# Kernel tuning notes

Measured on AMD Instinct MI355X. Metric: run time of the kernel, lower is better.

Reference implementation:

```python
import jax, jax.numpy as jnp
import numpy as np

NEG_SLOPE = 0.2  # LeakyReLU negative slope (act_negative)


def setup_inputs() -> dict:
    key = jax.random.key(0)
    ks = jax.random.split(key, 5)
    B, N, D = 64, 4096, 16
    x = jax.random.normal(ks[0], (B, N, D), dtype=jnp.float32)
    # random adjacency, scaled so row sums are O(1) and activations stay stable
    adj = jax.random.uniform(ks[1], (N, N), dtype=jnp.float32) * (2.0 / N)
    Identity = jnp.eye(N, dtype=jnp.float32)
    W0 = jax.random.normal(ks[2], (D, D), dtype=jnp.float32) * (1.0 / np.sqrt(D))
    W1 = jax.random.normal(ks[3], (D, D), dtype=jnp.float32) * (1.0 / np.sqrt(D))
    W2 = jax.random.normal(ks[4], (D, D), dtype=jnp.float32) * (1.0 / np.sqrt(D))
    return {"x": x, "adj": adj, "Identity": Identity, "W0": W0, "W1": W1, "W2": W2}


def _gcn_layer(x, W, adj, I):
    # GCNConv: linear (no bias) -> leaky_relu -> batched adjacency matmul.
    # The same conv (same W) is applied with adj and with Identity, then summed.
    h = jax.nn.leaky_relu(jnp.einsum('bnd,de->bne', x, W), NEG_SLOPE)
    out_adj = jnp.einsum('nm,bmh->bnh', adj, h)  # replaces per-sample torch.mm loop
    out_id = jnp.einsum('nm,bmh->bnh', I, h)
    return out_adj + out_id


def reference(x, adj, Identity, W0, W1, W2):
    out = _gcn_layer(x, W0, adj, Identity)
    out = _gcn_layer(out, W1, adj, Identity)
    out = _gcn_layer(out, W2, adj, Identity)
    return out  # is_residual=False: no shortcut branch
```

## Files before the change

### kernel.cpp

```cpp
#include <hip/hip_runtime.h>
#include <stdint.h>


typedef float  f32x4  __attribute__((ext_vector_type(4)));
typedef unsigned short ushort8 __attribute__((ext_vector_type(8)));
typedef int    i32x4  __attribute__((ext_vector_type(4)));
typedef int    i32x8  __attribute__((ext_vector_type(8)));

typedef __attribute__((address_space(1))) void* as1p;
typedef __attribute__((address_space(3))) void* as3p;
#define GLOAD_LDS16(G, L) \
  __builtin_amdgcn_global_load_lds((as1p)(G), (as3p)(L), 16, 0, 0)

#define P_ELEMS 4194304
#define ADJ_SCALE 4096.0f
#define ADJ_DESCALE (1.0f / 4096.0f)
#define SCALE_ONE 0x7f7f7f7f

__device__ __forceinline__ unsigned short f2bf(float f) {
  unsigned u = __float_as_uint(f);
  u += 0x7fffu + ((u >> 16) & 1u);
  return (unsigned short)(u >> 16);
}
__device__ __forceinline__ float bf2f(unsigned short u) {
  return __uint_as_float(((unsigned)u) << 16);
}
__device__ __forceinline__ int pk4_fp8(float a, float b, float c, float d) {
  int v = __builtin_amdgcn_cvt_pk_fp8_f32(a, b, 0, false);
  v = __builtin_amdgcn_cvt_pk_fp8_f32(c, d, v, true);
  return v;
}

__global__ void prep(const float* __restrict__ adj,
                     unsigned char* __restrict__ a8,
                     const float* __restrict__ x,
                     const float* __restrict__ W,
                     unsigned char* __restrict__ hb8,
                     unsigned short* __restrict__ hnc_out) {
  __shared__ float xs[64 * 65];
  __shared__ unsigned short ht[64 * 72];
  int bid = blockIdx.x;

  if (bid >= 1024) {
    size_t base = ((size_t)(bid - 1024) * 256 + threadIdx.x) * 16;
    const float4* src = (const float4*)(adj + base);
    float4 q0 = src[0], q1 = src[1], q2 = src[2], q3 = src[3];
    int4 o;
    o.x = pk4_fp8(q0.x * ADJ_SCALE, q0.y * ADJ_SCALE, q0.z * ADJ_SCALE, q0.w * ADJ_SCALE);
    o.y = pk4_fp8(q1.x * ADJ_SCALE, q1.y * ADJ_SCALE, q1.z * ADJ_SCALE, q1.w * ADJ_SCALE);
    o.z = pk4_fp8(q2.x * ADJ_SCALE, q2.y * ADJ_SCALE, q2.z * ADJ_SCALE, q2.w * ADJ_SCALE);
    o.w = pk4_fp8(q3.x * ADJ_SCALE, q3.y * ADJ_SCALE, q3.z * ADJ_SCALE, q3.w * ADJ_SCALE);
    *(int4*)(a8 + base) = o;
    return;
  }

  int n0 = (bid & 63) * 64, c0 = (bid >> 6) * 64;

  for (int i = threadIdx.x; i < 1024; i += 256) {
    int bs = i >> 8, rem = i & 255, nr = rem >> 2, d4 = rem & 3;
    float4 v = *(const float4*)(
        x + ((size_t)(c0 / 16 + bs) * 4096 + n0 + nr) * 16 + d4 * 4);
    float* dst = xs + nr * 65 + bs * 16 + d4 * 4;
    dst[0] = v.x; dst[1] = v.y; dst[2] = v.z; dst[3] = v.w;
  }
  __syncthreads();

  int n_l = threadIdx.x & 63, b_l = threadIdx.x >> 6;
  float xv[16];
#pragma unroll
  for (int d = 0; d < 16; ++d) xv[d] = xs[n_l * 65 + b_l * 16 + d];
  float accv[16];
#pragma unroll
  for (int e = 0; e < 16; ++e) accv[e] = 0.f;
#pragma unroll
  for (int d = 0; d < 16; ++d)
#pragma unroll
    for (int e = 0; e < 16; ++e) accv[e] += xv[d] * W[d * 16 + e];

  ushort8 h0, h1;
#pragma unroll
  for (int e = 0; e < 16; ++e) {
    float a = accv[e] > 0.f ? accv[e] : 0.2f * accv[e];
    unsigned short hv = f2bf(a);
    ht[(b_l * 16 + e) * 72 + n_l] = hv;
    if (e < 8) h0[e] = hv; else h1[e - 8] = hv;
  }
  unsigned short* ho = hnc_out + (size_t)(n0 + n_l) * 1024 + c0 + b_l * 16;
  *(ushort8*)(ho)     = h0;
  *(ushort8*)(ho + 8) = h1;
  __syncthreads();

  for (int i = threadIdx.x; i < 512; i += 256) {
    int row = i >> 3, ch = i & 7;
    const unsigned short* s = ht + row * 72 + ch * 8;
    int2 v;
    v.x = pk4_fp8(bf2f(s[0]), bf2f(s[1]), bf2f(s[2]), bf2f(s[3]));
    v.y = pk4_fp8(bf2f(s[4]), bf2f(s[5]), bf2f(s[6]), bf2f(s[7]));
    *(int2*)(hb8 + (size_t)(c0 + row) * 4096 + n0 + ch * 8) = v;
  }
}

__global__ void linear_fuse(const unsigned short* __restrict__ pp,
                            const unsigned short* __restrict__ hnc_in,
                            const float* __restrict__ W,
                            unsigned char* __restrict__ hb8,
                            unsigned short* __restrict__ hnc_out) {
  __shared__ float xs[64 * 65];
  __shared__ unsigned short ht[64 * 72];
  int n0 = blockIdx.x * 64, c0 = blockIdx.y * 64;

  for (int i = threadIdx.x; i < 512; i += 256) {
    int row = i >> 3, ch = i & 7;
    size_t g = (size_t)(n0 + row) * 1024 + c0 + ch * 8;
    ushort8 a = *(const ushort8*)(pp + g);
    ushort8 b = *(const ushort8*)(pp + P_ELEMS + g);
    ushort8 c = *(const ushort8*)(hnc_in + g);
    float* dst = xs + row * 65 + ch * 8;
#pragma unroll
    for (int j = 0; j < 8; ++j) dst[j] = bf2f(a[j]) + bf2f(b[j]) + bf2f(c[j]);
  }
  __syncthreads();

  int n_l = threadIdx.x & 63, b_l = threadIdx.x >> 6;
  float xv[16];
#pragma unroll
  for (int d = 0; d < 16; ++d) xv[d] = xs[n_l * 65 + b_l * 16 + d];
  float accv[16];
#pragma unroll
  for (int e = 0; e < 16; ++e) accv[e] = 0.f;
#pragma unroll
  for (int d = 0; d < 16; ++d)
#pragma unroll
    for (int e = 0; e < 16; ++e) accv[e] += xv[d] * W[d * 16 + e];

  ushort8 h0, h1;
#pragma unroll
  for (int e = 0; e < 16; ++e) {
    float a = accv[e] > 0.f ? accv[e] : 0.2f * accv[e];
    unsigned short hv = f2bf(a);
    ht[(b_l * 16 + e) * 72 + n_l] = hv;
    if (e < 8) h0[e] = hv; else h1[e - 8] = hv;
  }
  unsigned short* ho = hnc_out + (size_t)(n0 + n_l) * 1024 + c0 + b_l * 16;
  *(ushort8*)(ho)     = h0;
  *(ushort8*)(ho + 8) = h1;
  __syncthreads();

  for (int i = threadIdx.x; i < 512; i += 256) {
    int row = i >> 3, ch = i & 7;
    const unsigned short* s = ht + row * 72 + ch * 8;
    int2 v;
    v.x = pk4_fp8(bf2f(s[0]), bf2f(s[1]), bf2f(s[2]), bf2f(s[3]));
    v.y = pk4_fp8(bf2f(s[4]), bf2f(s[5]), bf2f(s[6]), bf2f(s[7]));
    *(int2*)(hb8 + (size_t)(c0 + row) * 4096 + n0 + ch * 8) = v;
  }
}

__global__ void add_out(const unsigned short* __restrict__ pp,
                        const unsigned short* __restrict__ hnc,
                        float* __restrict__ out) {
  int gid = blockIdx.x * 256 + threadIdx.x;
  int n = gid >> 7, c8 = (gid & 127) * 8;
  size_t g = (size_t)n * 1024 + c8;
  ushort8 a = *(const ushort8*)(pp + g);
  ushort8 b = *(const ushort8*)(pp + P_ELEMS + g);
  ushort8 h = *(const ushort8*)(hnc + g);
  float v[8];
#pragma unroll
  for (int j = 0; j < 8; ++j) v[j] = bf2f(a[j]) + bf2f(b[j]) + bf2f(h[j]);
  int bb = c8 >> 4, d0 = c8 & 15;
  float* o = out + (size_t)bb * 65536 + n * 16 + d0;
  *(float4*)(o)     = float4{v[0], v[1], v[2], v[3]};
  *(float4*)(o + 4) = float4{v[4], v[5], v[6], v[7]};
}

__global__ __launch_bounds__(256, 2)
void gemm_f8(const unsigned char* __restrict__ A,
             const unsigned char* __restrict__ B8,
             unsigned short* __restrict__ pp) {
  const int K = 4096;
  __shared__ unsigned char a_s[128 * 128];
  __shared__ unsigned char b_s[128 * 128];

  int tid = threadIdx.x, wave = tid >> 6, lane = tid & 63;

  int lin = blockIdx.x;
  int xcd = lin & 7, g = lin >> 3;
  int mth = g & 3, ct = (g >> 2) & 7, ks = g >> 5;
  int mt = mth * 8 + xcd;
  int n0 = mt * 128, c0 = ct * 128;
  int kbase = ks * 2048;

  int l8 = lane >> 3, lc = lane & 7;
  int swc = lc ^ l8;
  const unsigned char* gA[4];
  const unsigned char* gB[4];
#pragma unroll
  for (int j = 0; j < 4; ++j) {
    int r = wave * 32 + j * 8 + l8;
    gA[j] = A  + (size_t)(n0 + r) * K + kbase + swc * 16;
    gB[j] = B8 + (size_t)(c0 + r) * K + kbase + swc * 16;
  }

  int i16 = lane & 15, q = lane >> 4;
  int wm = wave >> 1, wn = wave & 1;
  int sw7 = i16 & 7;
  int pc0 = ((2 * q) ^ sw7) * 16;
  int pc1 = ((2 * q + 1) ^ sw7) * 16;

  f32x4 acc[4][4] = {};

  for (int it = 0; it < 16; ++it) {
    int k0 = it * 128;
    __syncthreads();
#pragma unroll
    for (int j = 0; j < 4; ++j) {
      GLOAD_LDS16(gA[j] + k0, a_s + (wave * 32 + j * 8) * 128);
      GLOAD_LDS16(gB[j] + k0, b_s + (wave * 32 + j * 8) * 128);
    }
    __syncthreads();

    i32x8 bv[4];
#pragma unroll
    for (int u = 0; u < 4; ++u) {
      const unsigned char* bp = b_s + (wn * 64 + u * 16 + i16) * 128;
      i32x4 blo = *(const i32x4*)(bp + pc0);
      i32x4 bhi = *(const i32x4*)(bp + pc1);
      bv[u] = __builtin_shufflevector(blo, bhi, 0, 1, 2, 3, 4, 5, 6, 7);
    }
#pragma unroll
    for (int t = 0; t < 4; ++t) {
      const unsigned char* ap = a_s + (wm * 64 + t * 16 + i16) * 128;
      i32x4 alo = *(const i32x4*)(ap + pc0);
      i32x4 ahi = *(const i32x4*)(ap + pc1);
      i32x8 av = __builtin_shufflevector(alo, ahi, 0, 1, 2, 3, 4, 5, 6, 7);
#pragma unroll
      for (int u = 0; u < 4; ++u)
        acc[t][u] = __builtin_amdgcn_mfma_scale_f32_16x16x128_f8f6f4(
            av, bv[u], acc[t][u], 0, 0, 0, SCALE_ONE, 0, SCALE_ONE);
    }
  }

  unsigned short* dst = pp + (size_t)ks * P_ELEMS;
#pragma unroll
  for (int t = 0; t < 4; ++t)
#pragma unroll
    for (int u = 0; u < 4; ++u)
#pragma unroll
      for (int i = 0; i < 4; ++i) {
        int n_g = n0 + wm * 64 + t * 16 + q * 4 + i;
        int c_g = c0 + wn * 64 + u * 16 + i16;
        dst[(size_t)n_g * 1024 + c_g] = f2bf(acc[t][u][i] * ADJ_DESCALE);
      }
}

extern "C" void kernel_launch(void* const* d_in, const int* in_sizes, int n_in,
                              void* d_out, int out_size, void* d_ws, size_t ws_size,
                              hipStream_t stream) {
  const float* x   = (const float*)d_in[0];
  const float* adj = (const float*)d_in[1];
  const float* W0  = (const float*)d_in[3];
  const float* W1  = (const float*)d_in[4];
  const float* W2  = (const float*)d_in[5];
  float* out = (float*)d_out;

  char* ws = (char*)d_ws;
  unsigned char*  adj8 = (unsigned char*)ws;
  unsigned char*  hb8  = (unsigned char*)(ws + 16777216);
  unsigned short* hnc  = (unsigned short*)(ws + 20971520);
  unsigned short* pp   = (unsigned short*)(ws + 29360128);

  prep<<<5120, 256, 0, stream>>>(adj, adj8, x, W0, hb8, hnc);
  gemm_f8<<<512, 256, 0, stream>>>(adj8, hb8, pp);
  linear_fuse<<<dim3(64, 16), 256, 0, stream>>>(pp, hnc, W1, hb8, hnc);
  gemm_f8<<<512, 256, 0, stream>>>(adj8, hb8, pp);
  linear_fuse<<<dim3(64, 16), 256, 0, stream>>>(pp, hnc, W2, hb8, hnc);
  gemm_f8<<<512, 256, 0, stream>>>(adj8, hb8, pp);
  add_out<<<2048, 256, 0, stream>>>(pp, hnc, out);
}
```

Before: 244.7 us.

## Double-buffer A tile in LDS and load B operands directly into registers

The FP8 GEMM now double-buffers the A tile in shared memory so the next k-slice is prefetched while the current one feeds the MFMAs. The B operand no longer goes through LDS; each lane loads its 32-byte fragment straight from global memory into registers, also one slice ahead. This removes one barrier per iteration and the B LDS round trip, so load latency can overlap compute. The cost is more registers for the two B fragment sets, and the direct B loads are narrower and less coalesced.

```diff
diff --git a/kernel.cpp b/kernel.cpp
--- a/kernel.cpp
+++ b/kernel.cpp
@@ -179,8 +179,7 @@
              const unsigned char* __restrict__ B8,
              unsigned short* __restrict__ pp) {
   const int K = 4096;
-  __shared__ unsigned char a_s[128 * 128];
-  __shared__ unsigned char b_s[128 * 128];
+  __shared__ unsigned char a_s[2][128 * 128];
 
   int tid = threadIdx.x, wave = tid >> 6, lane = tid & 63;
 
@@ -194,12 +193,10 @@
   int l8 = lane >> 3, lc = lane & 7;
   int swc = lc ^ l8;
   const unsigned char* gA[4];
-  const unsigned char* gB[4];
 #pragma unroll
   for (int j = 0; j < 4; ++j) {
     int r = wave * 32 + j * 8 + l8;
-    gA[j] = A  + (size_t)(n0 + r) * K + kbase + swc * 16;
-    gB[j] = B8 + (size_t)(c0 + r) * K + kbase + swc * 16;
+    gA[j] = A + (size_t)(n0 + r) * K + kbase + swc * 16;
   }
 
   int i16 = lane & 15, q = lane >> 4;
@@ -208,38 +205,67 @@
   int pc0 = ((2 * q) ^ sw7) * 16;
   int pc1 = ((2 * q + 1) ^ sw7) * 16;
 
+  const unsigned char* gB[4];
+#pragma unroll
+  for (int u = 0; u < 4; ++u)
+    gB[u] = B8 + (size_t)(c0 + wn * 64 + u * 16 + i16) * K + kbase + q * 32;
+
+#define STAGE_A(buf, k0)                                              \
+  do {                                                                \
+    _Pragma("unroll")                                                 \
+    for (int j = 0; j < 4; ++j)                                       \
+      GLOAD_LDS16(gA[j] + (k0), a_s[buf] + (wave * 32 + j * 8) * 128);\
+  } while (0)
+
+#define LOAD_B(dst, k0)                                               \
+  do {                                                                \
+    _Pragma("unroll")                                                 \
+    for (int u = 0; u < 4; ++u) {                                     \
+      const unsigned char* p = gB[u] + (k0);                          \
+      i32x4 lo = *(const i32x4*)p;                                    \
+      i32x4 hi = *(const i32x4*)(p + 16);                             \
+      dst[u] = __builtin_shufflevector(lo, hi, 0, 1, 2, 3, 4, 5, 6, 7); \
+    }                                                                 \
+  } while (0)
+
+#define COMPUTE(buf, bb)                                              \
+  do {                                                                \
+    _Pragma("unroll")                                                 \
+    for (int t = 0; t < 4; ++t) {                                     \
+      const unsigned char* ap = a_s[buf] + (wm * 64 + t * 16 + i16) * 128; \
+      i32x4 alo = *(const i32x4*)(ap + pc0);                          \
+      i32x4 ahi = *(const i32x4*)(ap + pc1);                          \
+      i32x8 av = __builtin_shufflevector(alo, ahi, 0, 1, 2, 3, 4, 5, 6, 7); \
+      _Pragma("unroll")                                               \
+      for (int u = 0; u < 4; ++u)                                     \
+        acc[t][u] = __builtin_amdgcn_mfma_scale_f32_16x16x128_f8f6f4( \
+            av, bb[u], acc[t][u], 0, 0, 0, SCALE_ONE, 0, SCALE_ONE);  \
+    }                                                                 \
+  } while (0)
+
   f32x4 acc[4][4] = {};
-
-  for (int it = 0; it < 16; ++it) {
-    int k0 = it * 128;
+  i32x8 b0[4], b1[4];
+
+  STAGE_A(0, 0);
+  LOAD_B(b0, 0);
+
+  for (int it = 0; it < 16; it += 2) {
     __syncthreads();
-#pragma unroll
-    for (int j = 0; j < 4; ++j) {
-      GLOAD_LDS16(gA[j] + k0, a_s + (wave * 32 + j * 8) * 128);
-      GLOAD_LDS16(gB[j] + k0, b_s + (wave * 32 + j * 8) * 128);
+    STAGE_A(1, (it + 1) * 128);
+    LOAD_B(b1, (it + 1) * 128);
+    COMPUTE(0, b0);
+
+    __syncthreads();
+    if (it + 2 < 16) {
+      STAGE_A(0, (it + 2) * 128);
+      LOAD_B(b0, (it + 2) * 128);
     }
-    __syncthreads();
-
-    i32x8 bv[4];
-#pragma unroll
-    for (int u = 0; u < 4; ++u) {
-      const unsigned char* bp = b_s + (wn * 64 + u * 16 + i16) * 128;
-      i32x4 blo = *(const i32x4*)(bp + pc0);
-      i32x4 bhi = *(const i32x4*)(bp + pc1);
-      bv[u] = __builtin_shufflevector(blo, bhi, 0, 1, 2, 3, 4, 5, 6, 7);
-    }
-#pragma unroll
-    for (int t = 0; t < 4; ++t) {
-      const unsigned char* ap = a_s + (wm * 64 + t * 16 + i16) * 128;
-      i32x4 alo = *(const i32x4*)(ap + pc0);
-      i32x4 ahi = *(const i32x4*)(ap + pc1);
-      i32x8 av = __builtin_shufflevector(alo, ahi, 0, 1, 2, 3, 4, 5, 6, 7);
-#pragma unroll
-      for (int u = 0; u < 4; ++u)
-        acc[t][u] = __builtin_amdgcn_mfma_scale_f32_16x16x128_f8f6f4(
-            av, bv[u], acc[t][u], 0, 0, 0, SCALE_ONE, 0, SCALE_ONE);
-    }
-  }
+    COMPUTE(1, b1);
+  }
+
+#undef STAGE_A
+#undef LOAD_B
+#undef COMPUTE
 
   unsigned short* dst = pp + (size_t)ks * P_ELEMS;
 #pragma unroll
```

New measurement: 298.1 us. +21.8%, slower.
